# Optimization experiments

Measured on AMD Instinct MI355X. Metric: run time of the kernel, lower is better.

The kernel has to match this reference:

```python
import jax, jax.numpy as jnp
import numpy as np

D_MODEL = 512
N_HEADS = 8
D_FF = 2048
WINDOW = 32
EPS = 1e-5


def _layernorm(x, g, b):
    mu = jnp.mean(x, axis=-1, keepdims=True)
    var = jnp.mean(jnp.square(x - mu), axis=-1, keepdims=True)
    return (x - mu) * jax.lax.rsqrt(var + EPS) * g + b


def setup_inputs() -> dict:
    key = jax.random.key(0)
    ks = jax.random.split(key, 12)
    B, S, D = 8, 8192, D_MODEL
    s = 0.02
    return {
        "x": jax.random.normal(ks[0], (B, S, D), dtype=jnp.float32),
        "Wq": jax.random.normal(ks[1], (D, D), dtype=jnp.float32) * s,
        "bq": jnp.zeros((D,), jnp.float32),
        "Wk": jax.random.normal(ks[2], (D, D), dtype=jnp.float32) * s,
        "bk": jnp.zeros((D,), jnp.float32),
        "Wv": jax.random.normal(ks[3], (D, D), dtype=jnp.float32) * s,
        "bv": jnp.zeros((D,), jnp.float32),
        "Wo": jax.random.normal(ks[4], (D, D), dtype=jnp.float32) * s,
        "bo": jnp.zeros((D,), jnp.float32),
        "g1": jnp.ones((D,), jnp.float32),
        "be1": jnp.zeros((D,), jnp.float32),
        "W1": jax.random.normal(ks[5], (D, D_FF), dtype=jnp.float32) * s,
        "b1": jnp.zeros((D_FF,), jnp.float32),
        "W2": jax.random.normal(ks[6], (D_FF, D), dtype=jnp.float32) * s,
        "b2": jnp.zeros((D,), jnp.float32),
        "g2": jnp.ones((D,), jnp.float32),
        "be2": jnp.zeros((D,), jnp.float32),
    }


def reference(x, Wq, bq, Wk, bk, Wv, bv, Wo, bo, g1, be1, W1, b1, W2, b2, g2, be2):
    B, S, D = x.shape
    H, W = N_HEADS, WINDOW
    dh = D // H
    nW = S // W

    def split(t):  # [B,S,D] -> [B,nW,W,H,dh]
        return t.reshape(B, nW, W, H, dh)

    q = split(x @ Wq + bq)
    k = split(x @ Wk + bk)
    v = split(x @ Wv + bv)

    # block-local (non-overlapping window) attention: [B,H,nW,W,W]
    scores = jnp.einsum('bnqhd,bnkhd->bhnqk', q, k) / jnp.sqrt(jnp.float32(dh))
    attn = jax.nn.softmax(scores, axis=-1)
    o = jnp.einsum('bhnqk,bnkhd->bnqhd', attn, v).reshape(B, S, D)
    attn_out = o @ Wo + bo

    x = _layernorm(x + attn_out, g1, be1)
    ff = jax.nn.relu(x @ W1 + b1) @ W2 + b2
    x = _layernorm(x + ff, g2, be2)
    return x
```

## Files before the change

kernel.cpp:

```cpp
#include <hip/hip_runtime.h>

typedef unsigned int uint;
typedef unsigned short ushort;

typedef __bf16 bf16x8 __attribute__((ext_vector_type(8)));
typedef float f32x4 __attribute__((ext_vector_type(4)));

__device__ __forceinline__ float bflo(uint u) { return __uint_as_float(u << 16); }
__device__ __forceinline__ float bfhi(uint u) { return __uint_as_float(u & 0xffff0000u); }
__device__ __forceinline__ ushort f2bf(float f) {
  uint u = __float_as_uint(f);
  u += 0x7fffu + ((u >> 16) & 1u);
  return (ushort)(u >> 16);
}
__device__ __forceinline__ uint pack2(float lo, float hi) {
  return (uint)f2bf(lo) | ((uint)f2bf(hi) << 16);
}

__global__ __launch_bounds__(256) void cvt_f32_bf16(
    const float* __restrict__ in, ushort* __restrict__ out)
{
  const long i = ((long)blockIdx.x * 256 + threadIdx.x) * 8;
  float4 a = *(const float4*)(in + i);
  float4 b = *(const float4*)(in + i + 4);
  uint4 r;
  r.x = pack2(a.x, a.y); r.y = pack2(a.z, a.w);
  r.z = pack2(b.x, b.y); r.w = pack2(b.z, b.w);
  *(uint4*)(out + i) = r;
}

__global__ __launch_bounds__(256) void transpose_wf(
    const float* __restrict__ in, ushort* __restrict__ out, int R, int Ccols)
{
  __shared__ float tile[32][33];
  const int tx = threadIdx.x, ty = threadIdx.y;
  const int c0 = blockIdx.x * 32, r0 = blockIdx.y * 32;
#pragma unroll
  for (int j = 0; j < 32; j += 8)
    tile[ty + j][tx] = in[(long)(r0 + ty + j) * Ccols + (c0 + tx)];
  __syncthreads();
#pragma unroll
  for (int j = 0; j < 32; j += 8)
    out[(long)(c0 + ty + j) * R + (r0 + tx)] = f2bf(tile[tx][ty + j]);
}

#define BM 128
#define BN 128
#define BKK 64

__global__ __launch_bounds__(256, 2) void gemm_bt(
    const ushort* __restrict__ A, const ushort* __restrict__ Bt,
    const float* __restrict__ bias, void* __restrict__ Cv,
    int M, int N, int K, int relu, int out_f32)
{
  __shared__ ushort As[BM * BKK];
  __shared__ ushort Bs[BN * BKK];
  const int t = threadIdx.x;
  const int w = t >> 6, l = t & 63;
  const int quad = l >> 4, l16 = l & 15;
  const int wm = w & 1, wn = w >> 1;
  const long m0 = (long)blockIdx.y * BM;
  const long n0 = (long)blockIdx.x * BN;

  const int srow = l >> 3;
  const int scol = (l & 7) * 8;

  f32x4 acc[4][4];
#pragma unroll
  for (int i = 0; i < 4; ++i)
#pragma unroll
    for (int j = 0; j < 4; ++j)
      acc[i][j] = f32x4{0.f, 0.f, 0.f, 0.f};

  for (int k0 = 0; k0 < K; k0 += BKK) {
#pragma unroll
    for (int i = 0; i < 4; ++i) {
      const int chunk = w * 4 + i;
      const int row = chunk * 8 + srow;
      const ushort* ga = A + (m0 + row) * (long)K + k0 + scol;
      const ushort* gb = Bt + (n0 + row) * (long)K + k0 + scol;
      __builtin_amdgcn_global_load_lds(
          (const __attribute__((address_space(1))) uint*)ga,
          (__attribute__((address_space(3))) uint*)(As + chunk * 512), 16, 0, 0);
      __builtin_amdgcn_global_load_lds(
          (const __attribute__((address_space(1))) uint*)gb,
          (__attribute__((address_space(3))) uint*)(Bs + chunk * 512), 16, 0, 0);
    }
    __syncthreads();
#pragma unroll
    for (int ks = 0; ks < 2; ++ks) {
      bf16x8 af[4], bfr[4];
#pragma unroll
      for (int im = 0; im < 4; ++im)
        af[im] = *(const bf16x8*)(As + (wm * 64 + im * 16 + l16) * BKK + ks * 32 + quad * 8);
#pragma unroll
      for (int in = 0; in < 4; ++in)
        bfr[in] = *(const bf16x8*)(Bs + (wn * 64 + in * 16 + l16) * BKK + ks * 32 + quad * 8);
#pragma unroll
      for (int im = 0; im < 4; ++im)
#pragma unroll
        for (int in = 0; in < 4; ++in)
          acc[im][in] = __builtin_amdgcn_mfma_f32_16x16x32_bf16(af[im], bfr[in], acc[im][in], 0, 0, 0);
    }
    __syncthreads();
  }

  ushort* Cb = (ushort*)Cv;
  float* Cf = (float*)Cv;
#pragma unroll
  for (int in = 0; in < 4; ++in) {
    const long col = n0 + wn * 64 + in * 16 + l16;
    const float bv = bias[col];
#pragma unroll
    for (int im = 0; im < 4; ++im) {
      const long row = m0 + wm * 64 + im * 16 + quad * 4;
#pragma unroll
      for (int r = 0; r < 4; ++r) {
        float vv = acc[im][in][r] + bv;
        if (relu) vv = fmaxf(vv, 0.f);
        if (out_f32) Cf[(row + r) * (long)N + col] = vv;
        else         Cb[(row + r) * (long)N + col] = f2bf(vv);
      }
    }
  }
}

__global__ __launch_bounds__(256, 2) void attn_mfma(
    ushort* qo, const ushort* __restrict__ k, const ushort* __restrict__ v)
{
  __shared__ ushort kv[32 * 512];
  __shared__ ushort pbuf[8][32 * 72];
  const int t = threadIdx.x;
  const int w = t >> 6, l = t & 63;
  const int quad = l >> 4, l16 = l & 15;
  const long base = (long)blockIdx.x * (32 * 512);

#pragma unroll
  for (int i = 0; i < 8; ++i) {
    const int c = w * 8 + i;
    __builtin_amdgcn_global_load_lds(
        (const __attribute__((address_space(1))) uint*)(k + base + c * 512 + l * 8),
        (__attribute__((address_space(3))) uint*)(kv + c * 512), 16, 0, 0);
  }
  bf16x8 qf[2][2][2];
#pragma unroll
  for (int hh = 0; hh < 2; ++hh) {
    const int h = w * 2 + hh;
#pragma unroll
    for (int mt = 0; mt < 2; ++mt)
#pragma unroll
      for (int ks = 0; ks < 2; ++ks)
        qf[hh][mt][ks] = *(const bf16x8*)(qo + base + (mt * 16 + l16) * 512 + h * 64 + ks * 32 + quad * 8);
  }
  __syncthreads();

#pragma unroll
  for (int hh = 0; hh < 2; ++hh) {
    const int h = w * 2 + hh;
    f32x4 sc[2][2];
#pragma unroll
    for (int mt = 0; mt < 2; ++mt)
#pragma unroll
      for (int nt = 0; nt < 2; ++nt)
        sc[mt][nt] = f32x4{0.f, 0.f, 0.f, 0.f};
#pragma unroll
    for (int ks = 0; ks < 2; ++ks) {
      bf16x8 kb0 = *(const bf16x8*)(kv + (0 * 16 + l16) * 512 + h * 64 + ks * 32 + quad * 8);
      bf16x8 kb1 = *(const bf16x8*)(kv + (1 * 16 + l16) * 512 + h * 64 + ks * 32 + quad * 8);
      sc[0][0] = __builtin_amdgcn_mfma_f32_16x16x32_bf16(qf[hh][0][ks], kb0, sc[0][0], 0, 0, 0);
      sc[0][1] = __builtin_amdgcn_mfma_f32_16x16x32_bf16(qf[hh][0][ks], kb1, sc[0][1], 0, 0, 0);
      sc[1][0] = __builtin_amdgcn_mfma_f32_16x16x32_bf16(qf[hh][1][ks], kb0, sc[1][0], 0, 0, 0);
      sc[1][1] = __builtin_amdgcn_mfma_f32_16x16x32_bf16(qf[hh][1][ks], kb1, sc[1][1], 0, 0, 0);
    }
    ushort* pb = pbuf[w * 2 + hh];
#pragma unroll
    for (int mt = 0; mt < 2; ++mt) {
#pragma unroll
      for (int r = 0; r < 4; ++r) {
        float a = sc[mt][0][r] * 0.125f;
        float b = sc[mt][1][r] * 0.125f;
        float mx = fmaxf(a, b);
        mx = fmaxf(mx, __shfl_xor(mx, 1));
        mx = fmaxf(mx, __shfl_xor(mx, 2));
        mx = fmaxf(mx, __shfl_xor(mx, 4));
        mx = fmaxf(mx, __shfl_xor(mx, 8));
        float ea = __expf(a - mx), eb = __expf(b - mx);
        float s = ea + eb;
        s += __shfl_xor(s, 1);
        s += __shfl_xor(s, 2);
        s += __shfl_xor(s, 4);
        s += __shfl_xor(s, 8);
        const float inv = 1.f / s;
        const int row = mt * 16 + quad * 4 + r;
        pb[row * 72 + 0 * 16 + l16] = f2bf(ea * inv);
        pb[row * 72 + 1 * 16 + l16] = f2bf(eb * inv);
      }
    }
  }
  __syncthreads();

#pragma unroll
  for (int i = 0; i < 8; ++i) {
    const int c = w * 8 + i;
    __builtin_amdgcn_global_load_lds(
        (const __attribute__((address_space(1))) uint*)(v + base + c * 512 + l * 8),
        (__attribute__((address_space(3))) uint*)(kv + c * 512), 16, 0, 0);
  }
  bf16x8 pf[2][2];
#pragma unroll
  for (int hh = 0; hh < 2; ++hh)
#pragma unroll
    for (int mt = 0; mt < 2; ++mt)
      pf[hh][mt] = *(const bf16x8*)(pbuf[w * 2 + hh] + (mt * 16 + l16) * 72 + quad * 8);
  __syncthreads();

#pragma unroll
  for (int hh = 0; hh < 2; ++hh) {
    const int h = w * 2 + hh;
    f32x4 oc[2][4];
#pragma unroll
    for (int mt = 0; mt < 2; ++mt)
#pragma unroll
      for (int nt = 0; nt < 4; ++nt)
        oc[mt][nt] = f32x4{0.f, 0.f, 0.f, 0.f};
#pragma unroll
    for (int nt = 0; nt < 4; ++nt) {
      bf16x8 bv;
#pragma unroll
      for (int j = 0; j < 8; ++j)
        bv[j] = ((const __bf16*)kv)[(quad * 8 + j) * 512 + h * 64 + nt * 16 + l16];
      oc[0][nt] = __builtin_amdgcn_mfma_f32_16x16x32_bf16(pf[hh][0], bv, oc[0][nt], 0, 0, 0);
      oc[1][nt] = __builtin_amdgcn_mfma_f32_16x16x32_bf16(pf[hh][1], bv, oc[1][nt], 0, 0, 0);
    }
    ushort* pb = pbuf[w * 2 + hh];
#pragma unroll
    for (int mt = 0; mt < 2; ++mt)
#pragma unroll
      for (int nt = 0; nt < 4; ++nt)
#pragma unroll
        for (int r = 0; r < 4; ++r)
          pb[(mt * 16 + quad * 4 + r) * 72 + nt * 16 + l16] = f2bf(oc[mt][nt][r]);
  }

#pragma unroll
  for (int i = 0; i < 8; ++i) {
    const int idx = i * 64 + l;
    const int hh = idx >> 8;
    const int row = (idx >> 3) & 31;
    const int c8 = idx & 7;
    uint4 d = *(const uint4*)(pbuf[w * 2 + hh] + row * 72 + c8 * 8);
    *(uint4*)(qo + base + row * 512 + (w * 2 + hh) * 64 + c8 * 8) = d;
  }
}

__global__ __launch_bounds__(256, 4) void ln1_res(
    const ushort* __restrict__ a, const ushort* __restrict__ b,
    const float* __restrict__ g, const float* __restrict__ be,
    ushort* __restrict__ out)
{
  const long row = (long)blockIdx.x * 4 + (threadIdx.x >> 6);
  const int lane = threadIdx.x & 63;
  const long off = row * 512 + lane * 8;
  uint4 ua = *(const uint4*)(a + off);
  uint4 ub = *(const uint4*)(b + off);
  float x[8];
  x[0] = bflo(ua.x) + bflo(ub.x); x[1] = bfhi(ua.x) + bfhi(ub.x);
  x[2] = bflo(ua.y) + bflo(ub.y); x[3] = bfhi(ua.y) + bfhi(ub.y);
  x[4] = bflo(ua.z) + bflo(ub.z); x[5] = bfhi(ua.z) + bfhi(ub.z);
  x[6] = bflo(ua.w) + bflo(ub.w); x[7] = bfhi(ua.w) + bfhi(ub.w);
  float sum = 0.f;
#pragma unroll
  for (int i = 0; i < 8; ++i) sum += x[i];
#pragma unroll
  for (int i = 1; i < 64; i <<= 1) sum += __shfl_xor(sum, i, 64);
  const float mu = sum * (1.0f / 512.0f);
  float vsum = 0.f;
#pragma unroll
  for (int i = 0; i < 8; ++i) { const float d = x[i] - mu; vsum += d * d; }
#pragma unroll
  for (int i = 1; i < 64; i <<= 1) vsum += __shfl_xor(vsum, i, 64);
  const float rs = rsqrtf(vsum * (1.0f / 512.0f) + 1e-5f);
  float4 g0 = *(const float4*)(g + lane * 8);
  float4 g1v = *(const float4*)(g + lane * 8 + 4);
  float4 e0 = *(const float4*)(be + lane * 8);
  float4 e1 = *(const float4*)(be + lane * 8 + 4);
  uint4 r;
  r.x = pack2((x[0] - mu) * rs * g0.x + e0.x, (x[1] - mu) * rs * g0.y + e0.y);
  r.y = pack2((x[2] - mu) * rs * g0.z + e0.z, (x[3] - mu) * rs * g0.w + e0.w);
  r.z = pack2((x[4] - mu) * rs * g1v.x + e1.x, (x[5] - mu) * rs * g1v.y + e1.y);
  r.w = pack2((x[6] - mu) * rs * g1v.z + e1.z, (x[7] - mu) * rs * g1v.w + e1.w);
  *(uint4*)(out + off) = r;
}

__global__ __launch_bounds__(256, 4) void ln2_res(
    const ushort* __restrict__ a, const float* bff,
    const float* __restrict__ g, const float* __restrict__ be,
    float* out)
{
  const long row = (long)blockIdx.x * 4 + (threadIdx.x >> 6);
  const int lane = threadIdx.x & 63;
  const long off = row * 512 + lane * 8;
  uint4 ua = *(const uint4*)(a + off);
  float4 fa = *(const float4*)(bff + off);
  float4 fb = *(const float4*)(bff + off + 4);
  float x[8];
  x[0] = bflo(ua.x) + fa.x; x[1] = bfhi(ua.x) + fa.y;
  x[2] = bflo(ua.y) + fa.z; x[3] = bfhi(ua.y) + fa.w;
  x[4] = bflo(ua.z) + fb.x; x[5] = bfhi(ua.z) + fb.y;
  x[6] = bflo(ua.w) + fb.z; x[7] = bfhi(ua.w) + fb.w;
  float sum = 0.f;
#pragma unroll
  for (int i = 0; i < 8; ++i) sum += x[i];
#pragma unroll
  for (int i = 1; i < 64; i <<= 1) sum += __shfl_xor(sum, i, 64);
  const float mu = sum * (1.0f / 512.0f);
  float vsum = 0.f;
#pragma unroll
  for (int i = 0; i < 8; ++i) { const float d = x[i] - mu; vsum += d * d; }
#pragma unroll
  for (int i = 1; i < 64; i <<= 1) vsum += __shfl_xor(vsum, i, 64);
  const float rs = rsqrtf(vsum * (1.0f / 512.0f) + 1e-5f);
  float4 g0 = *(const float4*)(g + lane * 8);
  float4 g1v = *(const float4*)(g + lane * 8 + 4);
  float4 e0 = *(const float4*)(be + lane * 8);
  float4 e1 = *(const float4*)(be + lane * 8 + 4);
  float4 r0, r1;
  r0.x = (x[0] - mu) * rs * g0.x + e0.x;
  r0.y = (x[1] - mu) * rs * g0.y + e0.y;
  r0.z = (x[2] - mu) * rs * g0.z + e0.z;
  r0.w = (x[3] - mu) * rs * g0.w + e0.w;
  r1.x = (x[4] - mu) * rs * g1v.x + e1.x;
  r1.y = (x[5] - mu) * rs * g1v.y + e1.y;
  r1.z = (x[6] - mu) * rs * g1v.z + e1.z;
  r1.w = (x[7] - mu) * rs * g1v.w + e1.w;
  *(float4*)(out + off) = r0;
  *(float4*)(out + off + 4) = r1;
}

extern "C" void kernel_launch(void* const* d_in, const int* in_sizes, int n_in,
                              void* d_out, int out_size, void* d_ws, size_t ws_size,
                              hipStream_t stream)
{
  const float* x   = (const float*)d_in[0];
  const float* Wq  = (const float*)d_in[1];
  const float* bq  = (const float*)d_in[2];
  const float* Wk  = (const float*)d_in[3];
  const float* bk  = (const float*)d_in[4];
  const float* Wv  = (const float*)d_in[5];
  const float* bv  = (const float*)d_in[6];
  const float* Wo  = (const float*)d_in[7];
  const float* bo  = (const float*)d_in[8];
  const float* g1  = (const float*)d_in[9];
  const float* be1 = (const float*)d_in[10];
  const float* W1  = (const float*)d_in[11];
  const float* b1  = (const float*)d_in[12];
  const float* W2  = (const float*)d_in[13];
  const float* b2  = (const float*)d_in[14];
  const float* g2  = (const float*)d_in[15];
  const float* be2 = (const float*)d_in[16];

  const long M = 65536;
  const size_t SZ = (size_t)M * 512;

  ushort* wsb = (ushort*)d_ws;
  ushort* xb  = wsb;
  ushort* R0  = wsb + SZ;
  ushort* Wqt = wsb + 2 * SZ;
  ushort* Wkt = Wqt + 512 * 512;
  ushort* Wvt = Wkt + 512 * 512;
  ushort* Wot = Wvt + 512 * 512;
  ushort* W1t = Wot + 512 * 512;
  ushort* W2t = W1t + 512 * 2048;

  ushort* outb = (ushort*)d_out;
  ushort* kb = outb;
  ushort* vb = outb + SZ;
  float* outf = (float*)d_out;

  dim3 tb(32, 8);
  transpose_wf<<<dim3(16, 16), tb, 0, stream>>>(Wq, Wqt, 512, 512);
  transpose_wf<<<dim3(16, 16), tb, 0, stream>>>(Wk, Wkt, 512, 512);
  transpose_wf<<<dim3(16, 16), tb, 0, stream>>>(Wv, Wvt, 512, 512);
  transpose_wf<<<dim3(16, 16), tb, 0, stream>>>(Wo, Wot, 512, 512);
  transpose_wf<<<dim3(64, 16), tb, 0, stream>>>(W1, W1t, 512, 2048);
  transpose_wf<<<dim3(16, 64), tb, 0, stream>>>(W2, W2t, 2048, 512);
  cvt_f32_bf16<<<dim3(16384), dim3(256), 0, stream>>>(x, xb);

  dim3 blk(256);
  gemm_bt<<<dim3(4, 512), blk, 0, stream>>>(xb, Wqt, bq, R0, 65536, 512, 512, 0, 0);
  gemm_bt<<<dim3(4, 512), blk, 0, stream>>>(xb, Wkt, bk, kb, 65536, 512, 512, 0, 0);
  gemm_bt<<<dim3(4, 512), blk, 0, stream>>>(xb, Wvt, bv, vb, 65536, 512, 512, 0, 0);
  attn_mfma<<<dim3(2048), blk, 0, stream>>>(R0, kb, vb);
  gemm_bt<<<dim3(4, 512), blk, 0, stream>>>(R0, Wot, bo, outb, 65536, 512, 512, 0, 0);
  ln1_res<<<dim3(16384), blk, 0, stream>>>(xb, outb, g1, be1, R0);
  for (int c = 0; c < 4; ++c) {
    const size_t rows0 = (size_t)c * 16384;
    gemm_bt<<<dim3(16, 128), blk, 0, stream>>>(R0 + rows0 * 512, W1t, b1, xb,
                                               16384, 2048, 512, 1, 0);
    gemm_bt<<<dim3(4, 128), blk, 0, stream>>>(xb, W2t, b2, outf + rows0 * 512,
                                              16384, 512, 2048, 0, 1);
  }
  ln2_res<<<dim3(16384), blk, 0, stream>>>(R0, outf, g2, be2, outf);
}
```

Baseline: 1.110 ms.

## Stage GEMM epilogue through LDS for vector stores and swizzle block order

The GEMM epilogue now writes accumulator tiles into padded shared memory and then issues coalesced 16-byte global stores for both the bf16 and fp32 outputs, instead of scattered 2- or 4-byte per-lane stores. The fp32 path is split into two halves so it fits in the reused LDS buffer. Workgroup IDs are also remapped across groups of 8 so that concurrently running blocks share A/B tiles in cache. The extra barriers and LDS traffic add epilogue latency, and the enlarged shared buffer may affect occupancy.

Result: faster. 1.038 ms (-6.5%).

```diff
diff --git a/kernel.cpp b/kernel.cpp
--- a/kernel.cpp
+++ b/kernel.cpp
@@ -47,20 +47,28 @@
 #define BM 128
 #define BN 128
 #define BKK 64
+#define CSTR 136
+#define FSTR 132
 
 __global__ __launch_bounds__(256, 2) void gemm_bt(
     const ushort* __restrict__ A, const ushort* __restrict__ Bt,
     const float* __restrict__ bias, void* __restrict__ Cv,
     int M, int N, int K, int relu, int out_f32)
 {
-  __shared__ ushort As[BM * BKK];
-  __shared__ ushort Bs[BN * BKK];
+  __shared__ ushort smem[17408];
+  ushort* As = smem;
+  ushort* Bs = smem + BM * BKK;
   const int t = threadIdx.x;
   const int w = t >> 6, l = t & 63;
   const int quad = l >> 4, l16 = l & 15;
   const int wm = w & 1, wn = w >> 1;
-  const long m0 = (long)blockIdx.y * BM;
-  const long n0 = (long)blockIdx.x * BN;
+
+  const int gx = gridDim.x;
+  int bid = blockIdx.y * gx + blockIdx.x;
+  const int nwg = gx * gridDim.y;
+  if ((nwg & 7) == 0) bid = (bid & 7) * (nwg >> 3) + (bid >> 3);
+  const long m0 = (long)(bid / gx) * BM;
+  const long n0 = (long)(bid % gx) * BN;
 
   const int srow = l >> 3;
   const int scol = (l & 7) * 8;
@@ -105,22 +113,63 @@
     __syncthreads();
   }
 
-  ushort* Cb = (ushort*)Cv;
-  float* Cf = (float*)Cv;
-#pragma unroll
-  for (int in = 0; in < 4; ++in) {
-    const long col = n0 + wn * 64 + in * 16 + l16;
-    const float bv = bias[col];
-#pragma unroll
-    for (int im = 0; im < 4; ++im) {
-      const long row = m0 + wm * 64 + im * 16 + quad * 4;
-#pragma unroll
-      for (int r = 0; r < 4; ++r) {
-        float vv = acc[im][in][r] + bv;
-        if (relu) vv = fmaxf(vv, 0.f);
-        if (out_f32) Cf[(row + r) * (long)N + col] = vv;
-        else         Cb[(row + r) * (long)N + col] = f2bf(vv);
+  if (!out_f32) {
+    ushort* Ct = smem;
+#pragma unroll
+    for (int in = 0; in < 4; ++in) {
+      const int cl = wn * 64 + in * 16 + l16;
+      const float bv = bias[n0 + cl];
+#pragma unroll
+      for (int im = 0; im < 4; ++im) {
+        const int rl = wm * 64 + im * 16 + quad * 4;
+#pragma unroll
+        for (int r = 0; r < 4; ++r) {
+          float vv = acc[im][in][r] + bv;
+          if (relu) vv = fmaxf(vv, 0.f);
+          Ct[(rl + r) * CSTR + cl] = f2bf(vv);
+        }
       }
+    }
+    __syncthreads();
+    ushort* Cb = (ushort*)Cv;
+#pragma unroll
+    for (int it = 0; it < 8; ++it) {
+      const int idx = it * 256 + t;
+      const int row = idx >> 4, c16 = idx & 15;
+      uint4 d = *(const uint4*)(Ct + row * CSTR + c16 * 8);
+      *(uint4*)(Cb + (m0 + row) * (long)N + n0 + c16 * 8) = d;
+    }
+  } else {
+    float* Cf4 = (float*)smem;
+    float* Cg = (float*)Cv;
+#pragma unroll
+    for (int half = 0; half < 2; ++half) {
+      if (wm == half) {
+#pragma unroll
+        for (int in = 0; in < 4; ++in) {
+          const int cl = wn * 64 + in * 16 + l16;
+          const float bv = bias[n0 + cl];
+#pragma unroll
+          for (int im = 0; im < 4; ++im) {
+            const int rl = im * 16 + quad * 4;
+#pragma unroll
+            for (int r = 0; r < 4; ++r) {
+              float vv = acc[im][in][r] + bv;
+              if (relu) vv = fmaxf(vv, 0.f);
+              Cf4[(rl + r) * FSTR + cl] = vv;
+            }
+          }
+        }
+      }
+      __syncthreads();
+#pragma unroll
+      for (int it = 0; it < 8; ++it) {
+        const int idx = it * 256 + t;
+        const int row = idx >> 5, c4 = idx & 31;
+        float4 d = *(const float4*)(Cf4 + row * FSTR + c4 * 4);
+        *(float4*)(Cg + (m0 + half * 64 + row) * (long)N + n0 + c4 * 4) = d;
+      }
+      __syncthreads();
     }
   }
 }
```
